# Kernel optimization log

Hardware: AMD Instinct MI355X
Metric: run time of the kernel (lower is better)

Reference implementation:

```python
import jax, jax.numpy as jnp
import numpy as np

B, S, DM, H = 8, 512, 1024, 16
D = DM // H            # head_dim = 64
NFEAT = 4              # len(feature_types)
N_DIST = 2 * 512 - 1   # max_utt_num*2-1 = 1023
N_DISC = 16 + 1        # len(DISCOURSE_RELATIONS)+1
N_COOC = 5 + 1


def setup_inputs() -> dict:
    key = jax.random.key(0)
    ks = jax.random.split(key, 24)
    inp = {}
    inp["query"] = jax.random.normal(ks[0], (B, S, DM), jnp.float32)
    inp["key"] = jax.random.normal(ks[1], (B, S, DM), jnp.float32)
    inp["value"] = jax.random.normal(ks[2], (B, S, DM), jnp.float32)
    inp["distance_adj"] = jax.random.randint(ks[3], (B, S, S), 0, N_DIST).astype(jnp.int32)
    inp["speaker_adj"] = jax.random.uniform(ks[4], (B, S, S), jnp.float32)
    inp["discourse_adj"] = jax.random.randint(ks[5], (B, S, S), 0, N_DISC).astype(jnp.int32)
    inp["cooccurrence_adj"] = jax.random.randint(ks[6], (B, S, S), 0, N_COOC).astype(jnp.int32)
    inp["mask"] = jnp.ones((B, 1, 1, S), jnp.int32)
    w = lambda k, shape: jax.random.normal(k, shape, jnp.float32) * 0.02
    inp["Wq"] = w(ks[7], (DM, DM)); inp["bq"] = jnp.zeros((DM,), jnp.float32)
    inp["Wk"] = w(ks[8], (DM, DM)); inp["bk"] = jnp.zeros((DM,), jnp.float32)
    inp["Wv"] = w(ks[9], (DM, DM)); inp["bv"] = jnp.zeros((DM,), jnp.float32)
    inp["Wo"] = w(ks[10], (DM, DM)); inp["bo"] = jnp.zeros((DM,), jnp.float32)
    inp["dist_embed"] = w(ks[11], (N_DIST, 1))
    inp["disc_embed"] = w(ks[12], (N_DISC, 1)).at[0].set(0.0)  # padding_idx=0
    inp["cooc_embed"] = w(ks[13], (N_COOC, 1)).at[0].set(0.0)  # padding_idx=0
    inp["fcw"] = w(ks[14], (H, NFEAT))       # per-head 1x1 conv weights
    inp["fcb"] = jnp.zeros((H,), jnp.float32)
    inp["cw"] = w(ks[15], (2,))              # combine conv weights
    inp["cb"] = jnp.zeros((), jnp.float32)
    return inp


def reference(query, key, value, distance_adj, speaker_adj, discourse_adj,
              cooccurrence_adj, mask, Wq, bq, Wk, bk, Wv, bv, Wo, bo,
              dist_embed, disc_embed, cooc_embed, fcw, fcb, cw, cb):
    scale = jnp.asarray(D ** 0.5, query.dtype)
    # Linear projections, split heads -> [B, H, S, D]
    split = lambda x: x.reshape(B, S, H, D).transpose(0, 2, 1, 3)
    Q = split(query @ Wq.T + bq)
    K = split(key @ Wk.T + bk)
    V = split(value @ Wv.T + bv)
    energy = jnp.einsum('bhqd,bhkd->bhqk', Q, K) / scale  # [B,H,S,S]
    # Adjacency feature maps in feature_types order: distance, speaker, discourse, cooccurrence
    dist = dist_embed[distance_adj, 0]
    disc = disc_embed[discourse_adj, 0] * (discourse_adj != 0)
    cooc = cooc_embed[cooccurrence_adj, 0] * (cooccurrence_adj != 0)
    feature_map = jnp.stack([dist, speaker_adj, disc, cooc], axis=1)  # [B,4,S,S]
    # Per-head 1x1 conv over the 4 feature channels + relu
    feat = jax.nn.relu(jnp.einsum('hc,bcij->bhij', fcw, feature_map)
                       + fcb[None, :, None, None])       # [B,H,S,S]
    # Combine conv (1x1, 2 channels -> 1) + relu
    energy = jax.nn.relu(cw[0] * energy + cw[1] * feat + cb)
    energy = jnp.where(mask == 0, -jnp.inf, energy)
    attention = jax.nn.softmax(energy, axis=-1)           # [B,H,S,S]
    x = jnp.einsum('bhqk,bhkd->bhqd', attention, V)       # dropout p=0 (eval)
    x = x.transpose(0, 2, 1, 3).reshape(B, S, DM)
    x = x @ Wo.T + bo
    return x, attention
```

## Files before the change

kernel.cpp:

```cpp
#include <hip/hip_runtime.h>

using short8 = __attribute__((ext_vector_type(8))) short;
using f32x4  = __attribute__((ext_vector_type(4))) float;
typedef unsigned short u16x4 __attribute__((ext_vector_type(4)));
typedef unsigned short u16x8 __attribute__((ext_vector_type(8)));

__device__ __forceinline__ unsigned short f2bf(float x) {
    union { float f; unsigned u; } v; v.f = x;
    unsigned u = v.u;
    unsigned r = (u + 0x7fffu + ((u >> 16) & 1u)) >> 16;
    return (unsigned short)r;
}
__device__ __forceinline__ float bf2f(unsigned short h) {
    union { unsigned u; float f; } v; v.u = ((unsigned)h) << 16;
    return v.f;
}

__device__ __forceinline__ void async16(const void* g, void* l) {
    __builtin_amdgcn_global_load_lds(
        (const __attribute__((address_space(1))) void*)g,
        (__attribute__((address_space(3))) void*)l, 16, 0, 0);
}

__device__ __forceinline__ short8 lds_swz8(const unsigned short* base, int row,
                                           int colbyte, int stride) {
    const char* p = (const char*)base + row * stride + (colbyte ^ ((row & 7) << 4));
    return *(const short8*)p;
}

__global__ __launch_bounds__(256) void cvt_all(
    const float* __restrict__ q, const float* __restrict__ k, const float* __restrict__ v,
    const float* __restrict__ wq, const float* __restrict__ wk,
    const float* __restrict__ wv, const float* __restrict__ wo,
    unsigned short* __restrict__ dstA, unsigned short* __restrict__ dstW)
{
    int bx = blockIdx.x;
    const float* src;
    unsigned short* o;
    size_t i;
    if (bx < 6144) {
        int z = bx >> 11;
        src = (z == 0) ? q : ((z == 1) ? k : v);
        o = dstA + (size_t)z * 4194304;
        i = ((size_t)(bx & 2047) * 256 + threadIdx.x) * 8;
    } else {
        int z = (bx - 6144) >> 9;
        src = (z == 0) ? wq : ((z == 1) ? wk : ((z == 2) ? wv : wo));
        o = dstW + (size_t)z * 1048576;
        i = ((size_t)((bx - 6144) & 511) * 256 + threadIdx.x) * 8;
    }
    float4 a = *(const float4*)(src + i);
    float4 b = *(const float4*)(src + i + 4);
    ushort4 lo, hi;
    lo.x = f2bf(a.x); lo.y = f2bf(a.y); lo.z = f2bf(a.z); lo.w = f2bf(a.w);
    hi.x = f2bf(b.x); hi.y = f2bf(b.y); hi.z = f2bf(b.z); hi.w = f2bf(b.w);
    *(ushort4*)(o + i) = lo;
    *(ushort4*)(o + i + 4) = hi;
}

__global__ __launch_bounds__(256) void feat_kernel(
    const int* __restrict__ dist_adj, const float* __restrict__ spk,
    const int* __restrict__ disc_adj, const int* __restrict__ cooc_adj,
    const float* __restrict__ dist_emb, const float* __restrict__ disc_emb,
    const float* __restrict__ cooc_emb, unsigned short* __restrict__ F)
{
    __shared__ float s_dist[1023];
    __shared__ float s_disc[17];
    __shared__ float s_cooc[6];
    int tid = threadIdx.x;
    for (int i = tid; i < 1023; i += 256) s_dist[i] = dist_emb[i];
    if (tid < 17) s_disc[tid] = disc_emb[tid];
    if (tid < 6)  s_cooc[tid] = cooc_emb[tid];
    __syncthreads();

    int bx = blockIdx.x;
    int k  = (bx & 1) * 256 + tid;
    int qq = (bx >> 1) & 127;
    int b  = bx >> 8;

    size_t abase = ((size_t)b * 512 + qq * 4) * 512 + k;
    u16x8 oA, oB;
#pragma unroll
    for (int r = 0; r < 4; ++r) {
        size_t a = abase + (size_t)r * 512;
        int dd   = __builtin_nontemporal_load(dist_adj + a);
        float sp = __builtin_nontemporal_load(spk + a);
        int dc   = __builtin_nontemporal_load(disc_adj + a);
        int cc   = __builtin_nontemporal_load(cooc_adj + a);
        unsigned short f0 = f2bf(s_dist[dd]);
        unsigned short f1 = f2bf(sp);
        unsigned short f2 = f2bf(dc ? s_disc[dc] : 0.f);
        unsigned short f3 = f2bf(cc ? s_cooc[cc] : 0.f);
        if (r < 2) {
            oA[r * 4 + 0] = f0; oA[r * 4 + 1] = f1; oA[r * 4 + 2] = f2; oA[r * 4 + 3] = f3;
        } else {
            oB[(r - 2) * 4 + 0] = f0; oB[(r - 2) * 4 + 1] = f1;
            oB[(r - 2) * 4 + 2] = f2; oB[(r - 2) * 4 + 3] = f3;
        }
    }
    unsigned short* fb = F + (((size_t)b * 128 + qq) * 512 + k) * 16;
    *(u16x8*)(fb)     = oA;
    *(u16x8*)(fb + 8) = oB;
}

template<int OMODE>
__device__ __forceinline__ void gemm_bf16_body(
    const unsigned short* __restrict__ A, const unsigned short* __restrict__ W,
    const float* __restrict__ bias, void* __restrict__ outp, int m0, int n0)
{
    __shared__ __align__(16) unsigned short As[128 * 32];
    __shared__ __align__(16) unsigned short Bs[128 * 32];
    int tid = threadIdx.x;
    int lane = tid & 63, wid = tid >> 6;
    int wx = wid & 1, wy = wid >> 1;
    int lanelo = lane & 15, hi8 = (lane >> 4) * 8;
    int rowc = lane >> 2;
    int colc = (lane & 3) * 8;

    f32x4 acc[4][4];
#pragma unroll
    for (int i = 0; i < 4; ++i)
#pragma unroll
        for (int j = 0; j < 4; ++j) {
            acc[i][j][0] = 0.f; acc[i][j][1] = 0.f; acc[i][j][2] = 0.f; acc[i][j][3] = 0.f;
        }

    for (int kk = 0; kk < 32; ++kk) {
        int k0 = kk * 32;
        __syncthreads();
#pragma unroll
        for (int p = 0; p < 2; ++p) {
            int c = 2 * wid + p;
            int row = c * 16 + rowc;
            async16(A + (size_t)(m0 + row) * 1024 + k0 + colc, As + c * 512);
        }
#pragma unroll
        for (int p = 0; p < 2; ++p) {
            int c = 2 * wid + p;
            int row = c * 16 + rowc;
            async16(W + (size_t)(n0 + row) * 1024 + k0 + colc, Bs + c * 512);
        }
        __syncthreads();

        short8 af[4], bfr[4];
#pragma unroll
        for (int i = 0; i < 4; ++i)
            af[i] = *(const short8*)(As + (wy*64 + i*16 + lanelo) * 32 + hi8);
#pragma unroll
        for (int j = 0; j < 4; ++j)
            bfr[j] = *(const short8*)(Bs + (wx*64 + j*16 + lanelo) * 32 + hi8);
#pragma unroll
        for (int i = 0; i < 4; ++i)
#pragma unroll
            for (int j = 0; j < 4; ++j)
                acc[i][j] = __builtin_amdgcn_mfma_f32_16x16x32_bf16(af[i], bfr[j], acc[i][j], 0, 0, 0);
    }

    float bia[4];
#pragma unroll
    for (int j = 0; j < 4; ++j) bia[j] = bias[n0 + wx*64 + j*16 + lanelo];
#pragma unroll
    for (int i = 0; i < 4; ++i) {
        int mbase = m0 + wy*64 + i*16 + (lane >> 4) * 4;
#pragma unroll
        for (int j = 0; j < 4; ++j) {
            int n = n0 + wx*64 + j*16 + lanelo;
#pragma unroll
            for (int r = 0; r < 4; ++r) {
                int m = mbase + r;
                float val = acc[i][j][r] + bia[j];
                if (OMODE == 0) {
                    unsigned short* o = (unsigned short*)outp;
                    o[((size_t)((m >> 9) * 16 + (n >> 6)) * 512 + (m & 511)) * 64 + (n & 63)] = f2bf(val);
                } else {
                    float* o = (float*)outp;
                    o[(size_t)m * 1024 + n] = val;
                }
            }
        }
    }
}

__global__ __launch_bounds__(256) void gemm_qkv(
    const unsigned short* __restrict__ Abf, const unsigned short* __restrict__ Wbf,
    const float* __restrict__ bq, const float* __restrict__ bk, const float* __restrict__ bv,
    unsigned short* Qb, unsigned short* Kb, unsigned short* Vb)
{
    int z = blockIdx.z;
    const unsigned short* A = Abf + (size_t)z * 4194304;
    const unsigned short* W = Wbf + (size_t)z * 1048576;
    const float* bias = (z == 0) ? bq : ((z == 1) ? bk : bv);
    unsigned short* o = (z == 0) ? Qb : ((z == 1) ? Kb : Vb);
    gemm_bf16_body<0>(A, W, bias, o, blockIdx.x * 128, blockIdx.y * 128);
}

__global__ __launch_bounds__(256) void gemm_proj(
    const unsigned short* __restrict__ xh, const unsigned short* __restrict__ Wo,
    const float* __restrict__ bo, float* __restrict__ out)
{
    gemm_bf16_body<1>(xh, Wo, bo, out, blockIdx.x * 128, blockIdx.y * 128);
}

__global__ __launch_bounds__(256) void transpose_v(const unsigned short* __restrict__ Vb,
                                                   unsigned short* __restrict__ Vt)
{
    __shared__ __align__(16) unsigned short T[64][72];
    int tid = threadIdx.x;
    int s0 = blockIdx.x * 64;
    int bh = blockIdx.z * 16 + blockIdx.y;
#pragma unroll
    for (int p = 0; p < 2; ++p) {
        int c = p * 256 + tid;
        int row = c >> 3, kc = (c & 7) * 8;
        uint4 v = *(const uint4*)(Vb + ((size_t)bh * 512 + s0 + row) * 64 + kc);
        *(uint4*)&T[row][kc] = v;
    }
    __syncthreads();
#pragma unroll
    for (int p = 0; p < 2; ++p) {
        int c = p * 256 + tid;
        int d = c >> 3, sc = (c & 7) * 8;
        unsigned vv[4];
#pragma unroll
        for (int i = 0; i < 4; ++i) {
            unsigned lo = T[sc + 2*i][d];
            unsigned hi = T[sc + 2*i + 1][d];
            vv[i] = lo | (hi << 16);
        }
        uint4 o; o.x = vv[0]; o.y = vv[1]; o.z = vv[2]; o.w = vv[3];
        *(uint4*)(Vt + ((size_t)bh * 64 + d) * 512 + s0 + sc) = o;
    }
}

__global__ __launch_bounds__(256, 2) void attn_kernel(
    const unsigned short* __restrict__ Qb, const unsigned short* __restrict__ Kb,
    const unsigned short* __restrict__ Vt, const unsigned short* __restrict__ F,
    const int* __restrict__ mask, const float* __restrict__ cw,
    const float* __restrict__ cb, const float* __restrict__ fcw,
    const float* __restrict__ fcb, float* __restrict__ attn_out,
    unsigned short* __restrict__ xh)
{
    __shared__ __align__(16) char smem[35840];
    unsigned short* Qs = (unsigned short*)smem;
    unsigned short* Ks = (unsigned short*)(smem + 8192);
    unsigned short* Vs = (unsigned short*)smem;
    unsigned short* Ps = (unsigned short*)(smem + 16384);
    int* s_mask = (int*)(smem + 33792);

    int tid = threadIdx.x;
    int lane = tid & 63, w = tid >> 6;
    int lanelo = lane & 15, hi8 = (lane >> 4) * 8;
    int hi2 = lane >> 4;

    int lin = blockIdx.x;
    int xcd = lin & 7;
    int s   = lin >> 3;
    int bh  = xcd * 16 + (s >> 3);
    int qt  = s & 7;
    int b   = bh >> 4, h = bh & 15;

    float qs  = cw[0] * 0.125f;
    float cw1 = cw[1];
    float cbv = cb[0];
    float w0 = fcw[h * 4 + 0], w1 = fcw[h * 4 + 1];
    float w2 = fcw[h * 4 + 2], w3 = fcw[h * 4 + 3];
    float fcb_h = fcb[h];

    s_mask[tid]       = mask[b * 512 + tid];
    s_mask[tid + 256] = mask[b * 512 + tid + 256];

    int r8  = lane >> 3;
    int gs8 = (lane & 7) ^ r8;
#pragma unroll
    for (int p = 0; p < 2; ++p) {
        int row = p * 32 + w * 8 + r8;
        async16(Qb + ((size_t)bh * 512 + qt * 64 + row) * 64 + gs8 * 8,
                Qs + (p * 32 + w * 8) * 64);
    }
    __syncthreads();

    short8 aq[2];
    aq[0] = lds_swz8(Qs, w * 16 + lanelo, hi8 * 2, 128);
    aq[1] = lds_swz8(Qs, w * 16 + lanelo, 64 + hi8 * 2, 128);
    int qrow = qt * 64 + w * 16 + hi2 * 4;
    int qq   = qt * 16 + w * 4 + hi2;
    const unsigned short* fbase = F + ((size_t)b * 128 + qq) * 512 * 16;

    float P[32][4];
#pragma unroll
    for (int kt = 0; kt < 4; ++kt) {
        const unsigned short* f0p = fbase + (size_t)(kt * 8 * 16 + lanelo) * 16;
        u16x8 fA = *(const u16x8*)(f0p);
        u16x8 fB = *(const u16x8*)(f0p + 8);
        __syncthreads();
#pragma unroll
        for (int p = 0; p < 4; ++p) {
            int row = p * 32 + w * 8 + r8;
            async16(Kb + ((size_t)bh * 512 + kt * 128 + row) * 64 + gs8 * 8,
                    Ks + (p * 32 + w * 8) * 64);
        }
        __syncthreads();
#pragma unroll
        for (int j = 0; j < 8; ++j) {
            int jn = (j < 7) ? j + 1 : 7;
            const unsigned short* fp = fbase + (size_t)((kt * 8 + jn) * 16 + lanelo) * 16;
            u16x8 fAn = *(const u16x8*)(fp);
            u16x8 fBn = *(const u16x8*)(fp + 8);
            short8 b0 = lds_swz8(Ks, j * 16 + lanelo, hi8 * 2, 128);
            short8 b1 = lds_swz8(Ks, j * 16 + lanelo, 64 + hi8 * 2, 128);
            f32x4 acc; acc[0] = 0.f; acc[1] = 0.f; acc[2] = 0.f; acc[3] = 0.f;
            acc = __builtin_amdgcn_mfma_f32_16x16x32_bf16(aq[0], b0, acc, 0, 0, 0);
            acc = __builtin_amdgcn_mfma_f32_16x16x32_bf16(aq[1], b1, acc, 0, 0, 0);
            int jj = kt * 8 + j;
            int kcol = jj * 16 + lanelo;
            int mk = s_mask[kcol];
#pragma unroll
            for (int r = 0; r < 4; ++r) {
                unsigned short e0, e1, e2, e3;
                if (r < 2) {
                    e0 = (unsigned short)fA[r*4+0]; e1 = (unsigned short)fA[r*4+1];
                    e2 = (unsigned short)fA[r*4+2]; e3 = (unsigned short)fA[r*4+3];
                } else {
                    e0 = (unsigned short)fB[(r-2)*4+0]; e1 = (unsigned short)fB[(r-2)*4+1];
                    e2 = (unsigned short)fB[(r-2)*4+2]; e3 = (unsigned short)fB[(r-2)*4+3];
                }
                float dot = w0 * bf2f(e0) + w1 * bf2f(e1) + w2 * bf2f(e2)
                          + w3 * bf2f(e3) + fcb_h;
                float gh = fmaxf(dot, 0.f) * cw1;
                float e = qs * acc[r] + gh + cbv;
                e = fmaxf(e, 0.f);
                P[jj][r] = mk ? __expf(e) : 0.f;
            }
            fA = fAn; fB = fBn;
        }
    }

    float inv[4];
#pragma unroll
    for (int r = 0; r < 4; ++r) {
        float s0 = 0.f;
#pragma unroll
        for (int jj = 0; jj < 32; ++jj) s0 += P[jj][r];
        s0 += __shfl_xor(s0, 1, 64);
        s0 += __shfl_xor(s0, 2, 64);
        s0 += __shfl_xor(s0, 4, 64);
        s0 += __shfl_xor(s0, 8, 64);
        inv[r] = 1.0f / s0;
    }

    {
        float* ap = attn_out + ((size_t)bh * 512 + qrow) * 512 + lanelo;
#pragma unroll
        for (int jj = 0; jj < 32; ++jj)
#pragma unroll
            for (int r = 0; r < 4; ++r)
                __builtin_nontemporal_store(P[jj][r] * inv[r],
                                            ap + (size_t)r * 512 + jj * 16);
    }

    f32x4 xacc[4];
#pragma unroll
    for (int jf = 0; jf < 4; ++jf) { xacc[jf][0]=0.f; xacc[jf][1]=0.f; xacc[jf][2]=0.f; xacc[jf][3]=0.f; }

    int r8v  = ((w & 1) * 4 + hi2) & 7;
    int gs16 = (lane & 15) ^ r8v;
    unsigned short* Psw = Ps + w * 16 * 136;
#pragma unroll
    for (int c = 0; c < 4; ++c) {
        __syncthreads();
#pragma unroll
        for (int p = 0; p < 4; ++p) {
            int row = p * 16 + w * 4 + hi2;
            async16(Vt + ((size_t)bh * 64 + row) * 512 + c * 128 + gs16 * 8,
                    Vs + (p * 16 + w * 4) * 128);
        }
#pragma unroll
        for (int jc = 0; jc < 8; ++jc) {
            int jj = c * 8 + jc;
#pragma unroll
            for (int r = 0; r < 4; ++r)
                Psw[(hi2 * 4 + r) * 136 + jc * 16 + lanelo] = f2bf(P[jj][r]);
        }
        __syncthreads();
#pragma unroll
        for (int ksub = 0; ksub < 4; ++ksub) {
            short8 ap8 = *(const short8*)(Psw + (size_t)lanelo * 136 + ksub * 32 + hi8);
#pragma unroll
            for (int jf = 0; jf < 4; ++jf) {
                short8 bv = lds_swz8(Vs, jf * 16 + lanelo, ksub * 64 + hi8 * 2, 256);
                xacc[jf] = __builtin_amdgcn_mfma_f32_16x16x32_bf16(ap8, bv, xacc[jf], 0, 0, 0);
            }
        }
    }

#pragma unroll
    for (int jf = 0; jf < 4; ++jf) {
        int d = jf * 16 + lanelo;
#pragma unroll
        for (int r = 0; r < 4; ++r) {
            float val = xacc[jf][r] * inv[r];
            xh[((size_t)b * 512 + qrow + r) * 1024 + h * 64 + d] = f2bf(val);
        }
    }
}

extern "C" void kernel_launch(void* const* d_in, const int* in_sizes, int n_in,
                              void* d_out, int out_size, void* d_ws, size_t ws_size,
                              hipStream_t stream) {
    (void)in_sizes; (void)n_in; (void)out_size; (void)ws_size;
    const float* query    = (const float*)d_in[0];
    const float* key      = (const float*)d_in[1];
    const float* value    = (const float*)d_in[2];
    const int*   dist_adj = (const int*)d_in[3];
    const float* spk      = (const float*)d_in[4];
    const int*   disc_adj = (const int*)d_in[5];
    const int*   cooc_adj = (const int*)d_in[6];
    const int*   maskp    = (const int*)d_in[7];
    const float* Wq = (const float*)d_in[8];  const float* bq = (const float*)d_in[9];
    const float* Wk = (const float*)d_in[10]; const float* bk = (const float*)d_in[11];
    const float* Wv = (const float*)d_in[12]; const float* bv = (const float*)d_in[13];
    const float* Wo = (const float*)d_in[14]; const float* bo = (const float*)d_in[15];
    const float* dist_emb = (const float*)d_in[16];
    const float* disc_emb = (const float*)d_in[17];
    const float* cooc_emb = (const float*)d_in[18];
    const float* fcw = (const float*)d_in[19];
    const float* fcb = (const float*)d_in[20];
    const float* cw  = (const float*)d_in[21];
    const float* cbp = (const float*)d_in[22];

    char* w = (char*)d_ws;
    unsigned short* Qb  = (unsigned short*)(w);
    unsigned short* Kb  = (unsigned short*)(w + 8388608);
    unsigned short* Vb  = (unsigned short*)(w + 16777216);
    unsigned short* Vt  = (unsigned short*)(w + 25165824);
    unsigned short* xh  = (unsigned short*)(w + 33554432);
    unsigned short* F   = (unsigned short*)(w + 41943040);
    unsigned short* Abf = (unsigned short*)(w + 41943040);
    unsigned short* Wbf = (unsigned short*)(w + 109051904);

    float* out_x    = (float*)d_out;
    float* attn_out = ((float*)d_out) + 4194304;

    cvt_all<<<dim3(8192, 1, 1), 256, 0, stream>>>(query, key, value, Wq, Wk, Wv, Wo,
                                                  Abf, Wbf);
    gemm_qkv<<<dim3(32, 8, 3), 256, 0, stream>>>(Abf, Wbf, bq, bk, bv, Qb, Kb, Vb);
    transpose_v<<<dim3(8, 16, 8), 256, 0, stream>>>(Vb, Vt);
    feat_kernel<<<2048, 256, 0, stream>>>(dist_adj, spk, disc_adj, cooc_adj,
                                          dist_emb, disc_emb, cooc_emb, F);
    attn_kernel<<<dim3(1024, 1, 1), 256, 0, stream>>>(Qb, Kb, Vt, F, maskp, cw, cbp,
                                                      fcw, fcb, attn_out, xh);
    gemm_proj<<<dim3(32, 8), 256, 0, stream>>>(xh, Wbf + 3145728, bo, out_x);
}
```

Baseline: 404.4 us.

## Recompute attention scores in a second pass instead of holding them in registers

The attention kernel no longer keeps the 32x4 score array in registers. A first pass computes only the row sums. A second pass recomputes QK^T and the feature term, normalizes, writes the attention output, and feeds the PV MFMA. This removes heavy register pressure and possible spills, which may also raise occupancy. The cost is doubled QK MFMA work, a second read of the feature tensor and K tiles, and LDS growing to about 51KB.

```diff
diff --git a/kernel.cpp b/kernel.cpp
--- a/kernel.cpp
+++ b/kernel.cpp
@@ -240,12 +240,12 @@
     const float* __restrict__ fcb, float* __restrict__ attn_out,
     unsigned short* __restrict__ xh)
 {
-    __shared__ __align__(16) char smem[35840];
+    __shared__ __align__(16) char smem[52224];
     unsigned short* Qs = (unsigned short*)smem;
-    unsigned short* Ks = (unsigned short*)(smem + 8192);
-    unsigned short* Vs = (unsigned short*)smem;
-    unsigned short* Ps = (unsigned short*)(smem + 16384);
-    int* s_mask = (int*)(smem + 33792);
+    unsigned short* Ks = (unsigned short*)smem;
+    unsigned short* Vs = (unsigned short*)(smem + 16384);
+    unsigned short* Ps = (unsigned short*)(smem + 32768);
+    int* s_mask = (int*)(smem + 50176);
 
     int tid = threadIdx.x;
     int lane = tid & 63, w = tid >> 6;
@@ -286,12 +286,9 @@
     int qq   = qt * 16 + w * 4 + hi2;
     const unsigned short* fbase = F + ((size_t)b * 128 + qq) * 512 * 16;
 
-    float P[32][4];
+    float ssum[4] = {0.f, 0.f, 0.f, 0.f};
 #pragma unroll
     for (int kt = 0; kt < 4; ++kt) {
-        const unsigned short* f0p = fbase + (size_t)(kt * 8 * 16 + lanelo) * 16;
-        u16x8 fA = *(const u16x8*)(f0p);
-        u16x8 fB = *(const u16x8*)(f0p + 8);
         __syncthreads();
 #pragma unroll
         for (int p = 0; p < 4; ++p) {
@@ -302,18 +299,15 @@
         __syncthreads();
 #pragma unroll
         for (int j = 0; j < 8; ++j) {
-            int jn = (j < 7) ? j + 1 : 7;
-            const unsigned short* fp = fbase + (size_t)((kt * 8 + jn) * 16 + lanelo) * 16;
-            u16x8 fAn = *(const u16x8*)(fp);
-            u16x8 fBn = *(const u16x8*)(fp + 8);
+            const unsigned short* fp = fbase + (size_t)((kt * 8 + j) * 16 + lanelo) * 16;
+            u16x8 fA = *(const u16x8*)(fp);
+            u16x8 fB = *(const u16x8*)(fp + 8);
             short8 b0 = lds_swz8(Ks, j * 16 + lanelo, hi8 * 2, 128);
             short8 b1 = lds_swz8(Ks, j * 16 + lanelo, 64 + hi8 * 2, 128);
             f32x4 acc; acc[0] = 0.f; acc[1] = 0.f; acc[2] = 0.f; acc[3] = 0.f;
             acc = __builtin_amdgcn_mfma_f32_16x16x32_bf16(aq[0], b0, acc, 0, 0, 0);
             acc = __builtin_amdgcn_mfma_f32_16x16x32_bf16(aq[1], b1, acc, 0, 0, 0);
-            int jj = kt * 8 + j;
-            int kcol = jj * 16 + lanelo;
-            int mk = s_mask[kcol];
+            int mk = s_mask[(kt * 8 + j) * 16 + lanelo];
 #pragma unroll
             for (int r = 0; r < 4; ++r) {
                 unsigned short e0, e1, e2, e3;
@@ -327,20 +321,16 @@
                 float dot = w0 * bf2f(e0) + w1 * bf2f(e1) + w2 * bf2f(e2)
                           + w3 * bf2f(e3) + fcb_h;
                 float gh = fmaxf(dot, 0.f) * cw1;
-                float e = qs * acc[r] + gh + cbv;
-                e = fmaxf(e, 0.f);
-                P[jj][r] = mk ? __expf(e) : 0.f;
+                float e = fmaxf(qs * acc[r] + gh + cbv, 0.f);
+                ssum[r] += mk ? __expf(e) : 0.f;
             }
-            fA = fAn; fB = fBn;
         }
     }
 
     float inv[4];
 #pragma unroll
     for (int r = 0; r < 4; ++r) {
-        float s0 = 0.f;
-#pragma unroll
-        for (int jj = 0; jj < 32; ++jj) s0 += P[jj][r];
+        float s0 = ssum[r];
         s0 += __shfl_xor(s0, 1, 64);
         s0 += __shfl_xor(s0, 2, 64);
         s0 += __shfl_xor(s0, 4, 64);
@@ -348,16 +338,6 @@
         inv[r] = 1.0f / s0;
     }
 
-    {
-        float* ap = attn_out + ((size_t)bh * 512 + qrow) * 512 + lanelo;
-#pragma unroll
-        for (int jj = 0; jj < 32; ++jj)
-#pragma unroll
-            for (int r = 0; r < 4; ++r)
-                __builtin_nontemporal_store(P[jj][r] * inv[r],
-                                            ap + (size_t)r * 512 + jj * 16);
-    }
-
     f32x4 xacc[4];
 #pragma unroll
     for (int jf = 0; jf < 4; ++jf) { xacc[jf][0]=0.f; xacc[jf][1]=0.f; xacc[jf][2]=0.f; xacc[jf][3]=0.f; }
@@ -365,21 +345,53 @@
     int r8v  = ((w & 1) * 4 + hi2) & 7;
     int gs16 = (lane & 15) ^ r8v;
     unsigned short* Psw = Ps + w * 16 * 136;
-#pragma unroll
-    for (int c = 0; c < 4; ++c) {
-        __syncthreads();
+    float* ap = attn_out + ((size_t)bh * 512 + qrow) * 512 + lanelo;
+
+#pragma unroll
+    for (int kt = 0; kt < 4; ++kt) {
+        __syncthreads();
+#pragma unroll
+        for (int p = 0; p < 4; ++p) {
+            int row = p * 32 + w * 8 + r8;
+            async16(Kb + ((size_t)bh * 512 + kt * 128 + row) * 64 + gs8 * 8,
+                    Ks + (p * 32 + w * 8) * 64);
+        }
 #pragma unroll
         for (int p = 0; p < 4; ++p) {
             int row = p * 16 + w * 4 + hi2;
-            async16(Vt + ((size_t)bh * 64 + row) * 512 + c * 128 + gs16 * 8,
+            async16(Vt + ((size_t)bh * 64 + row) * 512 + kt * 128 + gs16 * 8,
                     Vs + (p * 16 + w * 4) * 128);
         }
-#pragma unroll
-        for (int jc = 0; jc < 8; ++jc) {
-            int jj = c * 8 + jc;
-#pragma unroll
-            for (int r = 0; r < 4; ++r)
-                Psw[(hi2 * 4 + r) * 136 + jc * 16 + lanelo] = f2bf(P[jj][r]);
+        __syncthreads();
+#pragma unroll
+        for (int j = 0; j < 8; ++j) {
+            const unsigned short* fp = fbase + (size_t)((kt * 8 + j) * 16 + lanelo) * 16;
+            u16x8 fA = *(const u16x8*)(fp);
+            u16x8 fB = *(const u16x8*)(fp + 8);
+            short8 b0 = lds_swz8(Ks, j * 16 + lanelo, hi8 * 2, 128);
+            short8 b1 = lds_swz8(Ks, j * 16 + lanelo, 64 + hi8 * 2, 128);
+            f32x4 acc; acc[0] = 0.f; acc[1] = 0.f; acc[2] = 0.f; acc[3] = 0.f;
+            acc = __builtin_amdgcn_mfma_f32_16x16x32_bf16(aq[0], b0, acc, 0, 0, 0);
+            acc = __builtin_amdgcn_mfma_f32_16x16x32_bf16(aq[1], b1, acc, 0, 0, 0);
+            int mk = s_mask[(kt * 8 + j) * 16 + lanelo];
+#pragma unroll
+            for (int r = 0; r < 4; ++r) {
+                unsigned short e0, e1, e2, e3;
+                if (r < 2) {
+                    e0 = (unsigned short)fA[r*4+0]; e1 = (unsigned short)fA[r*4+1];
+                    e2 = (unsigned short)fA[r*4+2]; e3 = (unsigned short)fA[r*4+3];
+                } else {
+                    e0 = (unsigned short)fB[(r-2)*4+0]; e1 = (unsigned short)fB[(r-2)*4+1];
+                    e2 = (unsigned short)fB[(r-2)*4+2]; e3 = (unsigned short)fB[(r-2)*4+3];
+                }
+                float dot = w0 * bf2f(e0) + w1 * bf2f(e1) + w2 * bf2f(e2)
+                          + w3 * bf2f(e3) + fcb_h;
+                float gh = fmaxf(dot, 0.f) * cw1;
+                float e = fmaxf(qs * acc[r] + gh + cbv, 0.f);
+                float pn = mk ? __expf(e) * inv[r] : 0.f;
+                __builtin_nontemporal_store(pn, ap + (size_t)r * 512 + (kt * 8 + j) * 16);
+                Psw[(hi2 * 4 + r) * 136 + j * 16 + lanelo] = f2bf(pn);
+            }
         }
         __syncthreads();
 #pragma unroll
@@ -397,10 +409,8 @@
     for (int jf = 0; jf < 4; ++jf) {
         int d = jf * 16 + lanelo;
 #pragma unroll
-        for (int r = 0; r < 4; ++r) {
-            float val = xacc[jf][r] * inv[r];
-            xh[((size_t)b * 512 + qrow + r) * 1024 + h * 64 + d] = f2bf(val);
-        }
+        for (int r = 0; r < 4; ++r)
+            xh[((size_t)b * 512 + qrow + r) * 1024 + h * 64 + d] = f2bf(xacc[jf][r]);
     }
 }
 
```

Result: faster. 374.6 us (-7.4%).
